# Performance work log

Hardware: AMD Instinct MI355X
Metric: run time of the kernel (lower is better)

The kernel has to match this reference:

```python
import jax, jax.numpy as jnp
import numpy as np

LR = 0.01  # constraint relaxation learning rate (module default)
EPS = 1e-6


def setup_inputs() -> dict:
    key = jax.random.key(0)
    k1, k2, k3, k4 = jax.random.split(key, 4)
    N, E, K = 8192, 262144, 65536
    positions = jax.random.normal(k1, (N, 3), dtype=jnp.float32)
    edge_index = jax.random.randint(k2, (2, E), 0, N, dtype=jnp.int32)
    dist_idx = jax.random.randint(k3, (K, 2), 0, N, dtype=jnp.int32)
    dist_target = jax.random.uniform(k4, (K,), dtype=jnp.float32) * 2.0
    min_dist = jnp.ones((1,), dtype=jnp.float32) * 0.5
    return {"positions": positions, "edge_index": edge_index,
            "dist_idx": dist_idx, "dist_target": dist_target,
            "min_dist": min_dist}


def reference(positions, edge_index, dist_idx, dist_target, min_dist):
    x = positions  # (N, 3)
    N = x.shape[0]

    # --- distance constraints: ||x_i - x_j|| -> d_ij (Jacobi-style update) ---
    i, j = dist_idx[:, 0], dist_idx[:, 1]
    vec = x[i] - x[j]                                  # (K, 3)
    dist = jnp.sqrt(jnp.sum(vec * vec, axis=-1) + 1e-12)
    valid = (dist > EPS) & (i != j)
    coef = jnp.where(valid, LR * 0.5 * (dist - dist_target) / dist, 0.0)
    corr = coef[:, None] * vec                         # (K, 3)
    x = x.at[i].add(-corr).at[j].add(corr)

    # --- collision constraints: push apart all pairs with dist < min_dist ---
    md = min_dist[0]
    sq = jnp.sum(x * x, axis=-1)                       # (N,)
    d2 = jnp.maximum(sq[:, None] + sq[None, :] - 2.0 * (x @ x.T), 1e-12)
    dmat = jnp.sqrt(d2)                                # (N, N) pairwise distances
    mask = (dmat < md) & (dmat > EPS)                  # excludes diagonal (dist ~ 0)
    w = jnp.where(mask, (md - dmat) / dmat, 0.0) * (0.5 * LR)  # (N, N)
    # correction_i = sum_j w_ij * (x_i - x_j)
    x = x + x * jnp.sum(w, axis=-1, keepdims=True) - w @ x

    # --- gaussian curvature via normalized graph Laplacian ---
    e = jnp.clip(edge_index, 0, N - 1)
    adj = jnp.zeros((N, N), dtype=x.dtype).at[e[0], e[1]].set(1.0)
    adj = adj + adj.T
    deg = adj.sum(axis=1)
    dinv = jnp.where(deg == 0, 0.0, jnp.power(deg + EPS, -0.5))
    # L_norm @ x = x - D^{-1/2} A D^{-1/2} x (diagonal scaling, same math)
    lap = x - dinv[:, None] * (adj @ (dinv[:, None] * x))
    curvature = jnp.sqrt(jnp.sum(lap * lap, axis=-1) + 1e-12)  # (N,)

    return x, curvature
```

## Files before the change

kernel.cpp:

```cpp
#include <hip/hip_runtime.h>
#include <math.h>

#define N_NODES 8192
#define N3      24576
#define LR_C 0.01f
#define EPS_C 1e-6f
#define HASH_SLOTS (1u << 20)
#define HEMPTY 0xFFFFFFFFu
#define NB_SC 64
#define NB_DG 64
#define NB_LP 64

__global__ __launch_bounds__(512) void kA_corr_hashclear(
        const float* __restrict__ x0, const int* __restrict__ dist_idx,
        const float* __restrict__ dist_target,
        float* __restrict__ corr_part, uint4* __restrict__ hash4, int K) {
    __shared__ __align__(16) float smf[N3];
    int bid = blockIdx.x, tid = threadIdx.x;
    if (bid < NB_SC) {
        for (int t = tid; t < N3; t += 512) smf[t] = 0.f;
        __syncthreads();
        int per = (K + NB_SC - 1) / NB_SC;
        int base = bid * per;
        for (int kk = tid; kk < per; kk += 512) {
            int k = base + kk;
            if (k >= K) break;
            int i = dist_idx[2 * k], j = dist_idx[2 * k + 1];
            float ax = x0[3 * i], ay = x0[3 * i + 1], az = x0[3 * i + 2];
            float bx = x0[3 * j], by = x0[3 * j + 1], bz = x0[3 * j + 2];
            float vx = ax - bx, vy = ay - by, vz = az - bz;
            float dist = sqrtf(vx * vx + vy * vy + vz * vz + 1e-12f);
            bool valid = (dist > EPS_C) && (i != j);
            float coef = valid ? (LR_C * 0.5f) * (dist - dist_target[k]) / dist
                               : 0.0f;
            if (coef != 0.0f) {
                float cx = coef * vx, cy = coef * vy, cz = coef * vz;
                atomicAdd(&smf[3 * i],     -cx);
                atomicAdd(&smf[3 * i + 1], -cy);
                atomicAdd(&smf[3 * i + 2], -cz);
                atomicAdd(&smf[3 * j],      cx);
                atomicAdd(&smf[3 * j + 1],  cy);
                atomicAdd(&smf[3 * j + 2],  cz);
            }
        }
        __syncthreads();
        float* dst = corr_part + (size_t)bid * N3;
        for (int t = tid; t < N3; t += 512) dst[t] = smf[t];
    } else {
        int base = (bid - NB_SC) * 1024;
        hash4[base + tid]       = make_uint4(HEMPTY, HEMPTY, HEMPTY, HEMPTY);
        hash4[base + tid + 512] = make_uint4(HEMPTY, HEMPTY, HEMPTY, HEMPTY);
    }
}

__global__ __launch_bounds__(256) void kB_x1_hashflags(
        const float* __restrict__ pos, const float* __restrict__ corr_part,
        float* __restrict__ x1, const int* __restrict__ edge_index,
        unsigned int* __restrict__ hash, unsigned char* __restrict__ flags,
        int E) {
    int bid = blockIdx.x, tid = threadIdx.x;
    if (bid < 96) {
        int e = bid * 256 + tid;
        float s = pos[e];
        #pragma unroll 8
        for (int q = 0; q < NB_SC; ++q) s += corr_part[(size_t)q * N3 + e];
        x1[e] = s;
    } else {
        int k = (bid - 96) * 256 + tid;
        if (k >= E) return;
        int a = edge_index[k];
        int b = edge_index[E + k];
        a = min(max(a, 0), N_NODES - 1);
        b = min(max(b, 0), N_NODES - 1);
        unsigned int key = ((unsigned)a << 13) | (unsigned)b;
        unsigned int h = (key * 2654435761u) >> 12;
        bool unique = false;
        while (true) {
            unsigned int old = atomicCAS(&hash[h], HEMPTY, key);
            if (old == HEMPTY) { unique = true; break; }
            if (old == key)    { break; }
            h = (h + 1) & (HASH_SLOTS - 1);
        }
        flags[k] = unique ? 1 : 0;
    }
}

__global__ __launch_bounds__(256) void kC_rep_deg(
        const float* __restrict__ x1, const float* __restrict__ min_dist,
        float4* __restrict__ rep_part, const int* __restrict__ edge_index,
        const unsigned char* __restrict__ flags, int* __restrict__ deg_part,
        int E) {
    __shared__ __align__(16) unsigned char smu[32768];
    int bid = blockIdx.x, tid = threadIdx.x;
    if (bid < 512) {
        float4* pj = (float4*)smu;
        int ic = bid >> 5;
        int jc = bid & 31;
        int jbase = jc << 8;
        {
            int j = jbase + tid;
            float a = x1[3 * j], b = x1[3 * j + 1], c = x1[3 * j + 2];
            pj[tid] = make_float4(a, b, c, a * a + b * b + c * c);
        }
        __syncthreads();
        int i0 = (ic << 9) + tid;
        int i1 = i0 + 256;
        float x0v = x1[3 * i0], y0v = x1[3 * i0 + 1], z0v = x1[3 * i0 + 2];
        float x1v = x1[3 * i1], y1v = x1[3 * i1 + 1], z1v = x1[3 * i1 + 2];
        float sq0 = x0v * x0v + y0v * y0v + z0v * z0v;
        float sq1 = x1v * x1v + y1v * y1v + z1v * z1v;
        float md = min_dist[0];
        const float c0 = 0.5f * LR_C;
        float c1 = c0 * md;
        int di0 = i0 - jbase, di1 = i1 - jbase;
        float S0 = 0.f, ax0 = 0.f, ay0 = 0.f, az0 = 0.f;
        float S1 = 0.f, ax1 = 0.f, ay1 = 0.f, az1 = 0.f;
        #pragma unroll 4
        for (int jj = 0; jj < 256; ++jj) {
            float4 q = pj[jj];
            float dot0 = fmaf(x0v, q.x, fmaf(y0v, q.y, z0v * q.z));
            float d20 = fmaf(-2.0f, dot0, sq0 + q.w);
            float r0 = __builtin_amdgcn_rsqf(fmaxf(d20, 1e-12f));
            float w0 = fmaxf(fmaf(c1, r0, -c0), 0.0f);
            w0 = (d20 > 1e-12f && jj != di0) ? w0 : 0.0f;
            S0 += w0;
            ax0 = fmaf(w0, q.x, ax0); ay0 = fmaf(w0, q.y, ay0); az0 = fmaf(w0, q.z, az0);
            float dot1 = fmaf(x1v, q.x, fmaf(y1v, q.y, z1v * q.z));
            float d21 = fmaf(-2.0f, dot1, sq1 + q.w);
            float r1 = __builtin_amdgcn_rsqf(fmaxf(d21, 1e-12f));
            float w1 = fmaxf(fmaf(c1, r1, -c0), 0.0f);
            w1 = (d21 > 1e-12f && jj != di1) ? w1 : 0.0f;
            S1 += w1;
            ax1 = fmaf(w1, q.x, ax1); ay1 = fmaf(w1, q.y, ay1); az1 = fmaf(w1, q.z, az1);
        }
        rep_part[(size_t)jc * N_NODES + i0] = make_float4(ax0, ay0, az0, S0);
        rep_part[(size_t)jc * N_NODES + i1] = make_float4(ax1, ay1, az1, S1);
    } else {
        int* hist = (int*)smu;
        for (int t = tid; t < N_NODES; t += 256) hist[t] = 0;
        __syncthreads();
        int b = bid - 512;
        int per = (E + NB_DG - 1) / NB_DG;
        int base = b * per;
        for (int kk = tid; kk < per; kk += 256) {
            int k = base + kk;
            if (k >= E) break;
            if (!flags[k]) continue;
            int a = edge_index[k];
            int c = edge_index[E + k];
            a = min(max(a, 0), N_NODES - 1);
            c = min(max(c, 0), N_NODES - 1);
            atomicAdd(&hist[a], 1);
            atomicAdd(&hist[c], 1);
        }
        __syncthreads();
        int* dst = deg_part + (size_t)b * N_NODES;
        for (int t = tid; t < N_NODES; t += 256) dst[t] = hist[t];
    }
}

__global__ __launch_bounds__(256) void kD_finalize(
        const float* __restrict__ x1, const float4* __restrict__ rep_part,
        const int* __restrict__ deg_part,
        float* __restrict__ out_x, float4* __restrict__ z4) {
    int row = blockIdx.x * 256 + threadIdx.x;
    float S = 0.f, ax = 0.f, ay = 0.f, az = 0.f;
    #pragma unroll 8
    for (int c = 0; c < 32; ++c) {
        float4 q = rep_part[(size_t)c * N_NODES + row];
        ax += q.x; ay += q.y; az += q.z; S += q.w;
    }
    int d = 0;
    #pragma unroll 8
    for (int q = 0; q < NB_DG; ++q) d += deg_part[(size_t)q * N_NODES + row];
    float xi = x1[3 * row], yi = x1[3 * row + 1], zi = x1[3 * row + 2];
    float ox = xi + xi * S - ax;
    float oy = yi + yi * S - ay;
    float oz = zi + zi * S - az;
    out_x[3 * row] = ox; out_x[3 * row + 1] = oy; out_x[3 * row + 2] = oz;
    float dv = (d == 0) ? 0.0f : 1.0f / sqrtf((float)d + EPS_C);
    z4[row] = make_float4(dv * ox, dv * oy, dv * oz, dv);
}

__global__ __launch_bounds__(512) void kE_lap_hist(
        const int* __restrict__ edge_index, const unsigned char* __restrict__ flags,
        const float4* __restrict__ z4, float* __restrict__ lap_part, int E) {
    __shared__ __align__(16) float acc[N3];
    int bid = blockIdx.x, tid = threadIdx.x;
    for (int t = tid; t < N3; t += 512) acc[t] = 0.f;
    __syncthreads();
    int per = (E + NB_LP - 1) / NB_LP;
    int base = bid * per;
    for (int kk = tid; kk < per; kk += 512) {
        int k = base + kk;
        if (k >= E) break;
        if (!flags[k]) continue;
        int a = edge_index[k];
        int c = edge_index[E + k];
        a = min(max(a, 0), N_NODES - 1);
        c = min(max(c, 0), N_NODES - 1);
        float4 zc = z4[c];
        float4 za = z4[a];
        atomicAdd(&acc[3 * a],     zc.x);
        atomicAdd(&acc[3 * a + 1], zc.y);
        atomicAdd(&acc[3 * a + 2], zc.z);
        atomicAdd(&acc[3 * c],     za.x);
        atomicAdd(&acc[3 * c + 1], za.y);
        atomicAdd(&acc[3 * c + 2], za.z);
    }
    __syncthreads();
    float* dst = lap_part + (size_t)bid * N3;
    for (int t = tid; t < N3; t += 512) dst[t] = acc[t];
}

__global__ __launch_bounds__(256) void kF_curvature(
        const float* __restrict__ out_x, const float4* __restrict__ z4,
        const float* __restrict__ lap_part, float* __restrict__ out_curv) {
    int row = blockIdx.x * 256 + threadIdx.x;
    float lx = 0.f, ly = 0.f, lz = 0.f;
    #pragma unroll 8
    for (int q = 0; q < NB_LP; ++q) {
        const float* src = lap_part + (size_t)q * N3 + 3 * row;
        lx += src[0]; ly += src[1]; lz += src[2];
    }
    float dv = z4[row].w;
    float Lx = out_x[3 * row]     - dv * lx;
    float Ly = out_x[3 * row + 1] - dv * ly;
    float Lz = out_x[3 * row + 2] - dv * lz;
    out_curv[row] = sqrtf(Lx * Lx + Ly * Ly + Lz * Lz + 1e-12f);
}

extern "C" void kernel_launch(void* const* d_in, const int* in_sizes, int n_in,
                              void* d_out, int out_size, void* d_ws, size_t ws_size,
                              hipStream_t stream) {
    const float* positions   = (const float*)d_in[0];
    const int*   edge_index  = (const int*)d_in[1];
    const int*   dist_idx    = (const int*)d_in[2];
    const float* dist_target = (const float*)d_in[3];
    const float* min_dist    = (const float*)d_in[4];
    float* out = (float*)d_out;

    const int E = in_sizes[1] / 2;
    const int K = in_sizes[2] / 2;

    char* ws = (char*)d_ws;
    const size_t X1_OFF   = 0;
    const size_t Z4_OFF   = X1_OFF + (size_t)N3 * 4;
    const size_t FLAG_OFF = Z4_OFF + (size_t)N_NODES * 16;
    const size_t R1_OFF   = FLAG_OFF + (size_t)E;
    const size_t R2_OFF   = R1_OFF + (size_t)NB_SC * N3 * 4;

    float* x1            = (float*)(ws + X1_OFF);
    float4* z4           = (float4*)(ws + Z4_OFF);
    unsigned char* flags = (unsigned char*)(ws + FLAG_OFF);
    float* corr_part     = (float*)(ws + R1_OFF);
    float4* rep_part     = (float4*)(ws + R1_OFF);
    unsigned int* hash   = (unsigned int*)(ws + R2_OFF);
    int* deg_part        = (int*)(ws + R2_OFF + (size_t)HASH_SLOTS * 4);
    float* lap_part      = (float*)(ws + R2_OFF);

    kA_corr_hashclear<<<NB_SC + 256, 512, 0, stream>>>(
        positions, dist_idx, dist_target, corr_part, (uint4*)hash, K);

    kB_x1_hashflags<<<96 + (E + 255) / 256, 256, 0, stream>>>(
        positions, corr_part, x1, edge_index, hash, flags, E);

    kC_rep_deg<<<512 + NB_DG, 256, 0, stream>>>(
        x1, min_dist, rep_part, edge_index, flags, deg_part, E);

    kD_finalize<<<32, 256, 0, stream>>>(x1, rep_part, deg_part, out, z4);

    kE_lap_hist<<<NB_LP, 512, 0, stream>>>(edge_index, flags, z4, lap_part, E);

    kF_curvature<<<32, 256, 0, stream>>>(out, z4, lap_part, out + N3);
}
```

Before: 114.8 us.

## Replace hash-based edge dedup with per-row bitmask adjacency built in shared memory

Replaces the global atomicCAS hash table used to deduplicate edges with a dense adjacency bitmask. Each of 128 blocks scans all packed edges and sets bits for its 64 rows (both A and A^T) in shared memory, then takes degrees by popcount. The Laplacian and curvature pass then walks the set bits per row, which removes the degree and Laplacian partial buffers and their reduction kernels. The cost is that every scan block reads the full edge list, plus 16 MB of bitmask writes and later reads.

```diff
diff --git a/kernel.cpp b/kernel.cpp
--- a/kernel.cpp
+++ b/kernel.cpp
@@ -3,18 +3,19 @@
 
 #define N_NODES 8192
 #define N3      24576
+#define WPR     256
 #define LR_C 0.01f
 #define EPS_C 1e-6f
-#define HASH_SLOTS (1u << 20)
-#define HEMPTY 0xFFFFFFFFu
+#define NJ 32
 #define NB_SC 64
-#define NB_DG 64
-#define NB_LP 64
-
-__global__ __launch_bounds__(512) void kA_corr_hashclear(
+#define RPB 64
+#define NB_SCAN 128
+
+__global__ __launch_bounds__(512) void k1_corr_pack(
         const float* __restrict__ x0, const int* __restrict__ dist_idx,
-        const float* __restrict__ dist_target,
-        float* __restrict__ corr_part, uint4* __restrict__ hash4, int K) {
+        const float* __restrict__ dist_target, const int* __restrict__ edge_index,
+        float* __restrict__ corr_part, unsigned int* __restrict__ packed,
+        int K, int E) {
     __shared__ __align__(16) float smf[N3];
     int bid = blockIdx.x, tid = threadIdx.x;
     if (bid < NB_SC) {
@@ -47,187 +48,196 @@
         float* dst = corr_part + (size_t)bid * N3;
         for (int t = tid; t < N3; t += 512) dst[t] = smf[t];
     } else {
-        int base = (bid - NB_SC) * 1024;
-        hash4[base + tid]       = make_uint4(HEMPTY, HEMPTY, HEMPTY, HEMPTY);
-        hash4[base + tid + 512] = make_uint4(HEMPTY, HEMPTY, HEMPTY, HEMPTY);
-    }
-}
-
-__global__ __launch_bounds__(256) void kB_x1_hashflags(
+        int g = (bid - NB_SC) * 512 + tid;
+        const int4* a4 = (const int4*)edge_index;
+        const int4* b4 = (const int4*)(edge_index + E);
+        int4 a = a4[g];
+        int4 b = b4[g];
+        uint4 p;
+        p.x = ((unsigned)min(max(a.x, 0), N_NODES - 1) << 13) |
+               (unsigned)min(max(b.x, 0), N_NODES - 1);
+        p.y = ((unsigned)min(max(a.y, 0), N_NODES - 1) << 13) |
+               (unsigned)min(max(b.y, 0), N_NODES - 1);
+        p.z = ((unsigned)min(max(a.z, 0), N_NODES - 1) << 13) |
+               (unsigned)min(max(b.z, 0), N_NODES - 1);
+        p.w = ((unsigned)min(max(a.w, 0), N_NODES - 1) << 13) |
+               (unsigned)min(max(b.w, 0), N_NODES - 1);
+        ((uint4*)packed)[g] = p;
+    }
+}
+
+__global__ __launch_bounds__(512) void k3_scan(
+        const unsigned int* __restrict__ packed,
+        unsigned int* __restrict__ Ag, unsigned int* __restrict__ Bg,
+        int* __restrict__ deg,
         const float* __restrict__ pos, const float* __restrict__ corr_part,
-        float* __restrict__ x1, const int* __restrict__ edge_index,
-        unsigned int* __restrict__ hash, unsigned char* __restrict__ flags,
-        int E) {
-    int bid = blockIdx.x, tid = threadIdx.x;
-    if (bid < 96) {
-        int e = bid * 256 + tid;
+        float* __restrict__ x1, int E) {
+    __shared__ unsigned int mask[2 * RPB * WPR];
+    int bid = blockIdx.x, tid = threadIdx.x;
+    if (bid < NB_SCAN) {
+        for (int w = tid; w < 2 * RPB * WPR; w += 512) mask[w] = 0u;
+        __syncthreads();
+        int base = bid * RPB;
+        const uint4* p4 = (const uint4*)packed;
+        int n4 = E >> 2;
+        for (int it = tid; it < n4; it += 512) {
+            uint4 v = p4[it];
+            unsigned int vv[4] = { v.x, v.y, v.z, v.w };
+            #pragma unroll
+            for (int q = 0; q < 4; ++q) {
+                int a = vv[q] >> 13;
+                int b = vv[q] & (N_NODES - 1);
+                int ra = a - base;
+                if ((unsigned)ra < RPB)
+                    atomicOr(&mask[ra * WPR + (b >> 5)], 1u << (b & 31));
+                int rb = b - base;
+                if ((unsigned)rb < RPB)
+                    atomicOr(&mask[(RPB + rb) * WPR + (a >> 5)], 1u << (a & 31));
+            }
+        }
+        __syncthreads();
+        {
+            int r = tid >> 3, s = tid & 7;
+            int cnt = 0;
+            for (int w = s; w < WPR; w += 8) {
+                cnt += __popc(mask[r * WPR + w]);
+                cnt += __popc(mask[(RPB + r) * WPR + w]);
+            }
+            cnt += __shfl_down(cnt, 4, 8);
+            cnt += __shfl_down(cnt, 2, 8);
+            cnt += __shfl_down(cnt, 1, 8);
+            if (s == 0) deg[base + r] = cnt;
+        }
+        uint4* dstA = (uint4*)(Ag + (size_t)base * WPR);
+        uint4* dstB = (uint4*)(Bg + (size_t)base * WPR);
+        const uint4* sm4 = (const uint4*)mask;
+        int q4 = RPB * WPR / 4;
+        for (int w = tid; w < q4; w += 512) dstA[w] = sm4[w];
+        for (int w = tid; w < q4; w += 512) dstB[w] = sm4[q4 + w];
+    } else {
+        int e = (bid - NB_SCAN) * 512 + tid;
         float s = pos[e];
         #pragma unroll 8
         for (int q = 0; q < NB_SC; ++q) s += corr_part[(size_t)q * N3 + e];
         x1[e] = s;
-    } else {
-        int k = (bid - 96) * 256 + tid;
-        if (k >= E) return;
-        int a = edge_index[k];
-        int b = edge_index[E + k];
-        a = min(max(a, 0), N_NODES - 1);
-        b = min(max(b, 0), N_NODES - 1);
-        unsigned int key = ((unsigned)a << 13) | (unsigned)b;
-        unsigned int h = (key * 2654435761u) >> 12;
-        bool unique = false;
-        while (true) {
-            unsigned int old = atomicCAS(&hash[h], HEMPTY, key);
-            if (old == HEMPTY) { unique = true; break; }
-            if (old == key)    { break; }
-            h = (h + 1) & (HASH_SLOTS - 1);
-        }
-        flags[k] = unique ? 1 : 0;
-    }
-}
-
-__global__ __launch_bounds__(256) void kC_rep_deg(
+    }
+}
+
+__global__ __launch_bounds__(256) void k4_rep(
         const float* __restrict__ x1, const float* __restrict__ min_dist,
-        float4* __restrict__ rep_part, const int* __restrict__ edge_index,
-        const unsigned char* __restrict__ flags, int* __restrict__ deg_part,
-        int E) {
-    __shared__ __align__(16) unsigned char smu[32768];
-    int bid = blockIdx.x, tid = threadIdx.x;
-    if (bid < 512) {
-        float4* pj = (float4*)smu;
-        int ic = bid >> 5;
-        int jc = bid & 31;
-        int jbase = jc << 8;
-        {
-            int j = jbase + tid;
-            float a = x1[3 * j], b = x1[3 * j + 1], c = x1[3 * j + 2];
-            pj[tid] = make_float4(a, b, c, a * a + b * b + c * c);
-        }
-        __syncthreads();
-        int i0 = (ic << 9) + tid;
-        int i1 = i0 + 256;
-        float x0v = x1[3 * i0], y0v = x1[3 * i0 + 1], z0v = x1[3 * i0 + 2];
-        float x1v = x1[3 * i1], y1v = x1[3 * i1 + 1], z1v = x1[3 * i1 + 2];
-        float sq0 = x0v * x0v + y0v * y0v + z0v * z0v;
-        float sq1 = x1v * x1v + y1v * y1v + z1v * z1v;
-        float md = min_dist[0];
-        const float c0 = 0.5f * LR_C;
-        float c1 = c0 * md;
-        int di0 = i0 - jbase, di1 = i1 - jbase;
-        float S0 = 0.f, ax0 = 0.f, ay0 = 0.f, az0 = 0.f;
-        float S1 = 0.f, ax1 = 0.f, ay1 = 0.f, az1 = 0.f;
-        #pragma unroll 4
-        for (int jj = 0; jj < 256; ++jj) {
-            float4 q = pj[jj];
-            float dot0 = fmaf(x0v, q.x, fmaf(y0v, q.y, z0v * q.z));
-            float d20 = fmaf(-2.0f, dot0, sq0 + q.w);
-            float r0 = __builtin_amdgcn_rsqf(fmaxf(d20, 1e-12f));
-            float w0 = fmaxf(fmaf(c1, r0, -c0), 0.0f);
-            w0 = (d20 > 1e-12f && jj != di0) ? w0 : 0.0f;
-            S0 += w0;
-            ax0 = fmaf(w0, q.x, ax0); ay0 = fmaf(w0, q.y, ay0); az0 = fmaf(w0, q.z, az0);
-            float dot1 = fmaf(x1v, q.x, fmaf(y1v, q.y, z1v * q.z));
-            float d21 = fmaf(-2.0f, dot1, sq1 + q.w);
-            float r1 = __builtin_amdgcn_rsqf(fmaxf(d21, 1e-12f));
-            float w1 = fmaxf(fmaf(c1, r1, -c0), 0.0f);
-            w1 = (d21 > 1e-12f && jj != di1) ? w1 : 0.0f;
-            S1 += w1;
-            ax1 = fmaf(w1, q.x, ax1); ay1 = fmaf(w1, q.y, ay1); az1 = fmaf(w1, q.z, az1);
-        }
-        rep_part[(size_t)jc * N_NODES + i0] = make_float4(ax0, ay0, az0, S0);
-        rep_part[(size_t)jc * N_NODES + i1] = make_float4(ax1, ay1, az1, S1);
-    } else {
-        int* hist = (int*)smu;
-        for (int t = tid; t < N_NODES; t += 256) hist[t] = 0;
-        __syncthreads();
-        int b = bid - 512;
-        int per = (E + NB_DG - 1) / NB_DG;
-        int base = b * per;
-        for (int kk = tid; kk < per; kk += 256) {
-            int k = base + kk;
-            if (k >= E) break;
-            if (!flags[k]) continue;
-            int a = edge_index[k];
-            int c = edge_index[E + k];
-            a = min(max(a, 0), N_NODES - 1);
-            c = min(max(c, 0), N_NODES - 1);
-            atomicAdd(&hist[a], 1);
-            atomicAdd(&hist[c], 1);
-        }
-        __syncthreads();
-        int* dst = deg_part + (size_t)b * N_NODES;
-        for (int t = tid; t < N_NODES; t += 256) dst[t] = hist[t];
-    }
-}
-
-__global__ __launch_bounds__(256) void kD_finalize(
+        float4* __restrict__ rep_part) {
+    __shared__ __align__(16) float4 pj[256];
+    int bid = blockIdx.x, tid = threadIdx.x;
+    int ic = bid >> 5;
+    int jc = bid & 31;
+    int jbase = jc << 8;
+    {
+        int j = jbase + tid;
+        float a = x1[3 * j], b = x1[3 * j + 1], c = x1[3 * j + 2];
+        pj[tid] = make_float4(a, b, c, a * a + b * b + c * c);
+    }
+    __syncthreads();
+    int i0 = (ic << 9) + tid;
+    int i1 = i0 + 256;
+    float x0v = x1[3 * i0], y0v = x1[3 * i0 + 1], z0v = x1[3 * i0 + 2];
+    float x1v = x1[3 * i1], y1v = x1[3 * i1 + 1], z1v = x1[3 * i1 + 2];
+    float sq0 = x0v * x0v + y0v * y0v + z0v * z0v;
+    float sq1 = x1v * x1v + y1v * y1v + z1v * z1v;
+    float md = min_dist[0];
+    const float c0 = 0.5f * LR_C;
+    float c1 = c0 * md;
+    int di0 = i0 - jbase, di1 = i1 - jbase;
+    float S0 = 0.f, ax0 = 0.f, ay0 = 0.f, az0 = 0.f;
+    float S1 = 0.f, ax1 = 0.f, ay1 = 0.f, az1 = 0.f;
+    #pragma unroll 4
+    for (int jj = 0; jj < 256; ++jj) {
+        float4 q = pj[jj];
+        float dot0 = fmaf(x0v, q.x, fmaf(y0v, q.y, z0v * q.z));
+        float d20 = fmaf(-2.0f, dot0, sq0 + q.w);
+        float r0 = __builtin_amdgcn_rsqf(fmaxf(d20, 1e-12f));
+        float w0 = fmaxf(fmaf(c1, r0, -c0), 0.0f);
+        w0 = (d20 > 1e-12f && jj != di0) ? w0 : 0.0f;
+        S0 += w0;
+        ax0 = fmaf(w0, q.x, ax0); ay0 = fmaf(w0, q.y, ay0); az0 = fmaf(w0, q.z, az0);
+        float dot1 = fmaf(x1v, q.x, fmaf(y1v, q.y, z1v * q.z));
+        float d21 = fmaf(-2.0f, dot1, sq1 + q.w);
+        float r1 = __builtin_amdgcn_rsqf(fmaxf(d21, 1e-12f));
+        float w1 = fmaxf(fmaf(c1, r1, -c0), 0.0f);
+        w1 = (d21 > 1e-12f && jj != di1) ? w1 : 0.0f;
+        S1 += w1;
+        ax1 = fmaf(w1, q.x, ax1); ay1 = fmaf(w1, q.y, ay1); az1 = fmaf(w1, q.z, az1);
+    }
+    rep_part[(size_t)jc * N_NODES + i0] = make_float4(ax0, ay0, az0, S0);
+    rep_part[(size_t)jc * N_NODES + i1] = make_float4(ax1, ay1, az1, S1);
+}
+
+__global__ __launch_bounds__(256) void k5_finalize(
         const float* __restrict__ x1, const float4* __restrict__ rep_part,
-        const int* __restrict__ deg_part,
+        const int* __restrict__ deg,
         float* __restrict__ out_x, float4* __restrict__ z4) {
-    int row = blockIdx.x * 256 + threadIdx.x;
+    int gid = blockIdx.x * 256 + threadIdx.x;
+    int r = gid >> 3, s = gid & 7;
     float S = 0.f, ax = 0.f, ay = 0.f, az = 0.f;
-    #pragma unroll 8
-    for (int c = 0; c < 32; ++c) {
-        float4 q = rep_part[(size_t)c * N_NODES + row];
+    #pragma unroll
+    for (int c = s; c < NJ; c += 8) {
+        float4 q = rep_part[(size_t)c * N_NODES + r];
         ax += q.x; ay += q.y; az += q.z; S += q.w;
     }
-    int d = 0;
-    #pragma unroll 8
-    for (int q = 0; q < NB_DG; ++q) d += deg_part[(size_t)q * N_NODES + row];
-    float xi = x1[3 * row], yi = x1[3 * row + 1], zi = x1[3 * row + 2];
-    float ox = xi + xi * S - ax;
-    float oy = yi + yi * S - ay;
-    float oz = zi + zi * S - az;
-    out_x[3 * row] = ox; out_x[3 * row + 1] = oy; out_x[3 * row + 2] = oz;
-    float dv = (d == 0) ? 0.0f : 1.0f / sqrtf((float)d + EPS_C);
-    z4[row] = make_float4(dv * ox, dv * oy, dv * oz, dv);
-}
-
-__global__ __launch_bounds__(512) void kE_lap_hist(
-        const int* __restrict__ edge_index, const unsigned char* __restrict__ flags,
-        const float4* __restrict__ z4, float* __restrict__ lap_part, int E) {
-    __shared__ __align__(16) float acc[N3];
-    int bid = blockIdx.x, tid = threadIdx.x;
-    for (int t = tid; t < N3; t += 512) acc[t] = 0.f;
+    ax += __shfl_down(ax, 4, 8); ax += __shfl_down(ax, 2, 8); ax += __shfl_down(ax, 1, 8);
+    ay += __shfl_down(ay, 4, 8); ay += __shfl_down(ay, 2, 8); ay += __shfl_down(ay, 1, 8);
+    az += __shfl_down(az, 4, 8); az += __shfl_down(az, 2, 8); az += __shfl_down(az, 1, 8);
+    S  += __shfl_down(S, 4, 8);  S  += __shfl_down(S, 2, 8);  S  += __shfl_down(S, 1, 8);
+    if (s == 0) {
+        float xi = x1[3 * r], yi = x1[3 * r + 1], zi = x1[3 * r + 2];
+        float ox = xi + xi * S - ax;
+        float oy = yi + yi * S - ay;
+        float oz = zi + zi * S - az;
+        out_x[3 * r] = ox; out_x[3 * r + 1] = oy; out_x[3 * r + 2] = oz;
+        int d = deg[r];
+        float dv = (d == 0) ? 0.0f : 1.0f / sqrtf((float)d + EPS_C);
+        z4[r] = make_float4(dv * ox, dv * oy, dv * oz, dv);
+    }
+}
+
+__global__ __launch_bounds__(512) void k6_lap_curv(
+        const unsigned int* __restrict__ Ag, const unsigned int* __restrict__ Bg,
+        const float4* __restrict__ z4, const float* __restrict__ out_x,
+        float* __restrict__ out_curv) {
+    __shared__ float acc[RPB][4];
+    int bid = blockIdx.x, tid = threadIdx.x;
+    int base = bid * RPB;
+    if (tid < RPB) { acc[tid][0] = 0.f; acc[tid][1] = 0.f; acc[tid][2] = 0.f; }
     __syncthreads();
-    int per = (E + NB_LP - 1) / NB_LP;
-    int base = bid * per;
-    for (int kk = tid; kk < per; kk += 512) {
-        int k = base + kk;
-        if (k >= E) break;
-        if (!flags[k]) continue;
-        int a = edge_index[k];
-        int c = edge_index[E + k];
-        a = min(max(a, 0), N_NODES - 1);
-        c = min(max(c, 0), N_NODES - 1);
-        float4 zc = z4[c];
-        float4 za = z4[a];
-        atomicAdd(&acc[3 * a],     zc.x);
-        atomicAdd(&acc[3 * a + 1], zc.y);
-        atomicAdd(&acc[3 * a + 2], zc.z);
-        atomicAdd(&acc[3 * c],     za.x);
-        atomicAdd(&acc[3 * c + 1], za.y);
-        atomicAdd(&acc[3 * c + 2], za.z);
+    int nw = RPB * WPR;
+    for (int w = tid; w < nw; w += 512) {
+        int r = w >> 8;
+        int wi = w & (WPR - 1);
+        unsigned int m = Ag[(size_t)base * WPR + w];
+        while (m) {
+            int bit = __ffs(m) - 1; m &= m - 1;
+            float4 z = z4[wi * 32 + bit];
+            atomicAdd(&acc[r][0], z.x);
+            atomicAdd(&acc[r][1], z.y);
+            atomicAdd(&acc[r][2], z.z);
+        }
+        m = Bg[(size_t)base * WPR + w];
+        while (m) {
+            int bit = __ffs(m) - 1; m &= m - 1;
+            float4 z = z4[wi * 32 + bit];
+            atomicAdd(&acc[r][0], z.x);
+            atomicAdd(&acc[r][1], z.y);
+            atomicAdd(&acc[r][2], z.z);
+        }
     }
     __syncthreads();
-    float* dst = lap_part + (size_t)bid * N3;
-    for (int t = tid; t < N3; t += 512) dst[t] = acc[t];
-}
-
-__global__ __launch_bounds__(256) void kF_curvature(
-        const float* __restrict__ out_x, const float4* __restrict__ z4,
-        const float* __restrict__ lap_part, float* __restrict__ out_curv) {
-    int row = blockIdx.x * 256 + threadIdx.x;
-    float lx = 0.f, ly = 0.f, lz = 0.f;
-    #pragma unroll 8
-    for (int q = 0; q < NB_LP; ++q) {
-        const float* src = lap_part + (size_t)q * N3 + 3 * row;
-        lx += src[0]; ly += src[1]; lz += src[2];
-    }
-    float dv = z4[row].w;
-    float Lx = out_x[3 * row]     - dv * lx;
-    float Ly = out_x[3 * row + 1] - dv * ly;
-    float Lz = out_x[3 * row + 2] - dv * lz;
-    out_curv[row] = sqrtf(Lx * Lx + Ly * Ly + Lz * Lz + 1e-12f);
+    if (tid < RPB) {
+        int r = base + tid;
+        float dv = z4[r].w;
+        float Lx = out_x[3 * r]     - dv * acc[tid][0];
+        float Ly = out_x[3 * r + 1] - dv * acc[tid][1];
+        float Lz = out_x[3 * r + 2] - dv * acc[tid][2];
+        out_curv[r] = sqrtf(Lx * Lx + Ly * Ly + Lz * Lz + 1e-12f);
+    }
 }
 
 extern "C" void kernel_launch(void* const* d_in, const int* in_sizes, int n_in,
@@ -245,32 +255,32 @@
 
     char* ws = (char*)d_ws;
     const size_t X1_OFF   = 0;
-    const size_t Z4_OFF   = X1_OFF + (size_t)N3 * 4;
-    const size_t FLAG_OFF = Z4_OFF + (size_t)N_NODES * 16;
-    const size_t R1_OFF   = FLAG_OFF + (size_t)E;
-    const size_t R2_OFF   = R1_OFF + (size_t)NB_SC * N3 * 4;
+    const size_t Z4_OFF   = X1_OFF   + (size_t)N3 * 4;
+    const size_t DEG_OFF  = Z4_OFF   + (size_t)N_NODES * 16;
+    const size_t PACK_OFF = DEG_OFF  + (size_t)N_NODES * 4;
+    const size_t CORR_OFF = PACK_OFF + (size_t)E * 4;
+    const size_t REP_OFF  = CORR_OFF + (size_t)NB_SC * N3 * 4;
+    const size_t AG_OFF   = REP_OFF  + (size_t)NJ * N_NODES * 16;
+    const size_t BG_OFF   = AG_OFF   + (size_t)N_NODES * WPR * 4;
 
     float* x1            = (float*)(ws + X1_OFF);
     float4* z4           = (float4*)(ws + Z4_OFF);
-    unsigned char* flags = (unsigned char*)(ws + FLAG_OFF);
-    float* corr_part     = (float*)(ws + R1_OFF);
-    float4* rep_part     = (float4*)(ws + R1_OFF);
-    unsigned int* hash   = (unsigned int*)(ws + R2_OFF);
-    int* deg_part        = (int*)(ws + R2_OFF + (size_t)HASH_SLOTS * 4);
-    float* lap_part      = (float*)(ws + R2_OFF);
-
-    kA_corr_hashclear<<<NB_SC + 256, 512, 0, stream>>>(
-        positions, dist_idx, dist_target, corr_part, (uint4*)hash, K);
-
-    kB_x1_hashflags<<<96 + (E + 255) / 256, 256, 0, stream>>>(
-        positions, corr_part, x1, edge_index, hash, flags, E);
-
-    kC_rep_deg<<<512 + NB_DG, 256, 0, stream>>>(
-        x1, min_dist, rep_part, edge_index, flags, deg_part, E);
-
-    kD_finalize<<<32, 256, 0, stream>>>(x1, rep_part, deg_part, out, z4);
-
-    kE_lap_hist<<<NB_LP, 512, 0, stream>>>(edge_index, flags, z4, lap_part, E);
-
-    kF_curvature<<<32, 256, 0, stream>>>(out, z4, lap_part, out + N3);
-}
+    int*   deg           = (int*)(ws + DEG_OFF);
+    unsigned int* packed = (unsigned int*)(ws + PACK_OFF);
+    float* corr_part     = (float*)(ws + CORR_OFF);
+    float4* rep_part     = (float4*)(ws + REP_OFF);
+    unsigned int* Ag     = (unsigned int*)(ws + AG_OFF);
+    unsigned int* Bg     = (unsigned int*)(ws + BG_OFF);
+
+    k1_corr_pack<<<NB_SC + 128, 512, 0, stream>>>(
+        positions, dist_idx, dist_target, edge_index, corr_part, packed, K, E);
+
+    k3_scan<<<NB_SCAN + 48, 512, 0, stream>>>(
+        packed, Ag, Bg, deg, positions, corr_part, x1, E);
+
+    k4_rep<<<512, 256, 0, stream>>>(x1, min_dist, rep_part);
+
+    k5_finalize<<<256, 256, 0, stream>>>(x1, rep_part, deg, out, z4);
+
+    k6_lap_curv<<<NB_SCAN, 512, 0, stream>>>(Ag, Bg, z4, out, out + N3);
+}
```

Measured after the change: 159.0 us. 1.38x slower.
